# Kernel tuning notes

Hardware: AMD Instinct MI355X
Metric: run time of the kernel (lower is better)

## Reference

```python
import jax, jax.numpy as jnp
import numpy as np

D_MODEL = 1024
N_HEADS = 16
FEATURE_DIM = 16
HEAD_DIM = D_MODEL // N_HEADS  # 64
EPS = 1e-12


def taylor_exp(x):
    """2nd-order Taylor feature map of exp(q^T k / sqrt(d)).
    x: (b, h, l, d) -> (b, h, l, 1 + d + d^2)"""
    d = x.shape[-1]
    rd = jnp.sqrt(jnp.asarray(d, x.dtype))      # sqrt(d)
    rrd = jnp.sqrt(rd)                          # d^(1/4)
    r2 = jnp.sqrt(jnp.asarray(2.0, x.dtype))
    x2 = (x[..., :, None] * x[..., None, :]).reshape(*x.shape[:-1], d * d) / r2
    ones = jnp.ones_like(x[..., :1])
    return jnp.concatenate([ones, x / rrd, x2 / rd], axis=-1)


def setup_inputs() -> dict:
    key = jax.random.key(0)
    k0, k1, k2, k3, k4 = jax.random.split(key, 5)
    b, l = 1, 1024
    scale = 1.0 / np.sqrt(D_MODEL)
    hidden_states = jax.random.normal(k0, (b, l, D_MODEL), dtype=jnp.float32)
    Wq = jax.random.normal(k1, (N_HEADS * FEATURE_DIM, D_MODEL), dtype=jnp.float32) * scale
    Wk = jax.random.normal(k2, (N_HEADS * FEATURE_DIM, D_MODEL), dtype=jnp.float32) * scale
    Wv = jax.random.normal(k3, (N_HEADS * HEAD_DIM, D_MODEL), dtype=jnp.float32) * scale
    Wo = jax.random.normal(k4, (D_MODEL, N_HEADS * HEAD_DIM), dtype=jnp.float32) * scale
    return {"hidden_states": hidden_states, "Wq": Wq, "Wk": Wk, "Wv": Wv, "Wo": Wo}


def reference(hidden_states, Wq, Wk, Wv, Wo):
    b, l, _ = hidden_states.shape
    # projections (bias-free)
    q = (hidden_states @ Wq.T).reshape(b, l, N_HEADS, FEATURE_DIM).transpose(0, 2, 1, 3)
    k = (hidden_states @ Wk.T).reshape(b, l, N_HEADS, FEATURE_DIM).transpose(0, 2, 1, 3)
    v = (hidden_states @ Wv.T).reshape(b, l, N_HEADS, HEAD_DIM).transpose(0, 2, 1, 3)
    qf = taylor_exp(q)   # (b, h, l, D) with D = 1 + d + d^2 = 273
    kf = taylor_exp(k)
    # causal linear attention via associative KV accumulation
    # kv_state[l] = sum_{t<=l} phi(k_t) outer v_t  -> (b, h, l, head_dim, D)
    kv_state = jnp.cumsum(kf[..., None, :] * v[..., :, None], axis=2)
    num = jnp.einsum('bhlD,bhldD->bhld', qf, kv_state)
    den = jnp.einsum('bhlD,bhlD->bhl', qf, jnp.cumsum(kf, axis=2))[..., None] + EPS
    y = num / den                                # (b, h, l, head_dim)
    y = y.transpose(0, 2, 1, 3).reshape(b, l, N_HEADS * HEAD_DIM)
    return y @ Wo.T
```

## Files before the change

### kernel.cpp

```cpp
#include <hip/hip_runtime.h>

#define LSEQ 1024
#define DMODEL 1024
#define NHEADS 16
#define FDIM 16
#define HDIM 64
#define CHUNK 64
#define NCHUNK 16

typedef __attribute__((ext_vector_type(8))) short short8;
typedef __attribute__((ext_vector_type(4))) float floatx4;

__device__ __forceinline__ float bf2f(unsigned short u) {
    unsigned int x = ((unsigned int)u) << 16;
    return __builtin_bit_cast(float, x);
}
__device__ __forceinline__ unsigned short f2bf(float f) {
    unsigned int x = __builtin_bit_cast(unsigned int, f);
    unsigned int r = (x + 0x7fffu + ((x >> 16) & 1u)) >> 16;
    return (unsigned short)r;
}

__device__ __forceinline__ int block_detect_fp32(const unsigned short* wq) {
    __shared__ int cnt;
    if (threadIdx.x == 0) cnt = 0;
    __syncthreads();
    int bad = 0;
    for (int i = threadIdx.x; i < 1024; i += blockDim.x) {
        int e = (wq[i] >> 7) & 0xFF;
        if (e >= 143 || (e > 0 && e <= 80)) bad++;
    }
    if (bad) atomicAdd(&cnt, bad);
    __syncthreads();
    return cnt > 128;
}

#define U_QB   0
#define U_KB   262144
#define U_VB   524288
#define U_YB   1572864

#define MFMA(a, b, c) __builtin_amdgcn_mfma_f32_16x16x32_bf16((a), (b), (c), 0, 0, 0)

__device__ __forceinline__ void gemm64_body(
    unsigned short (&As)[64][136], unsigned short (&Bs)[64][136],
    const void* Araw, int a_fp32, int arow0,
    const void* Braw, int b_fp32, int brow0, floatx4 acc[4]) {
    int t = threadIdx.x;
    int r = t >> 2, c0 = (t & 3) * 32;
    int wave = t >> 6, lane = t & 63;
    int ml = lane & 15, q4 = lane >> 4;
    int mq = (wave >> 1) * 32, nq = (wave & 1) * 32;
    #pragma unroll
    for (int i = 0; i < 4; ++i) acc[i] = (floatx4){0.f, 0.f, 0.f, 0.f};

    short8 av[4], bv[4], av2[4], bv2[4];
    auto stage = [&](int k0, short8* a, short8* b) {
        if (!a_fp32) {
            const unsigned short* Ap = (const unsigned short*)Araw + (size_t)(arow0 + r) * DMODEL + k0 + c0;
            #pragma unroll
            for (int j = 0; j < 4; ++j) a[j] = *(const short8*)(Ap + j * 8);
        } else {
            const float* Ap = (const float*)Araw + (size_t)(arow0 + r) * DMODEL + k0 + c0;
            #pragma unroll
            for (int j = 0; j < 4; ++j)
                #pragma unroll
                for (int u = 0; u < 8; ++u) a[j][u] = (short)f2bf(Ap[j * 8 + u]);
        }
        if (!b_fp32) {
            const unsigned short* Bp = (const unsigned short*)Braw + (size_t)(brow0 + r) * DMODEL + k0 + c0;
            #pragma unroll
            for (int j = 0; j < 4; ++j) b[j] = *(const short8*)(Bp + j * 8);
        } else {
            const float* Bp = (const float*)Braw + (size_t)(brow0 + r) * DMODEL + k0 + c0;
            #pragma unroll
            for (int j = 0; j < 4; ++j)
                #pragma unroll
                for (int u = 0; u < 8; ++u) b[j][u] = (short)f2bf(Bp[j * 8 + u]);
        }
    };

    stage(0, av, bv);
    for (int k0 = 0; k0 < DMODEL; k0 += 128) {
        __syncthreads();
        #pragma unroll
        for (int j = 0; j < 4; ++j) {
            *(short8*)&As[r][c0 + j * 8] = av[j];
            *(short8*)&Bs[r][c0 + j * 8] = bv[j];
        }
        __syncthreads();
        if (k0 + 128 < DMODEL) stage(k0 + 128, av2, bv2);
        #pragma unroll
        for (int kk = 0; kk < 4; ++kk) {
            short8 a0 = *(const short8*)&As[mq + ml][kk * 32 + q4 * 8];
            short8 a1 = *(const short8*)&As[mq + 16 + ml][kk * 32 + q4 * 8];
            short8 b0 = *(const short8*)&Bs[nq + ml][kk * 32 + q4 * 8];
            short8 b1 = *(const short8*)&Bs[nq + 16 + ml][kk * 32 + q4 * 8];
            acc[0] = MFMA(a0, b0, acc[0]); acc[1] = MFMA(a0, b1, acc[1]);
            acc[2] = MFMA(a1, b0, acc[2]); acc[3] = MFMA(a1, b1, acc[3]);
        }
        #pragma unroll
        for (int j = 0; j < 4; ++j) { av[j] = av2[j]; bv[j] = bv2[j]; }
    }
}

__global__ __launch_bounds__(256) void qkv_gemm(
    const void* __restrict__ hidR, const void* __restrict__ WqR,
    const void* __restrict__ WkR, const void* __restrict__ WvR,
    unsigned short* __restrict__ qb, unsigned short* __restrict__ kb,
    unsigned short* __restrict__ vb) {
    int fp32 = block_detect_fp32((const unsigned short*)WqR);
    __shared__ __align__(16) unsigned short As[64][136];
    __shared__ __align__(16) unsigned short Bs[64][136];
    int nb = blockIdx.x, mb = blockIdx.y;
    const void* Braw; unsigned short* Cout; int ldc, col0, br0;
    if (nb < 4)      { Braw = WqR; br0 = nb * 64;       Cout = qb; ldc = 256;  col0 = nb * 64; }
    else if (nb < 8) { Braw = WkR; br0 = (nb - 4) * 64; Cout = kb; ldc = 256;  col0 = (nb - 4) * 64; }
    else             { Braw = WvR; br0 = (nb - 8) * 64; Cout = vb; ldc = 1024; col0 = (nb - 8) * 64; }

    floatx4 acc[4];
    gemm64_body(As, Bs, hidR, fp32, mb * 64, Braw, fp32, br0, acc);

    int wave = threadIdx.x >> 6, lane = threadIdx.x & 63;
    int ml = lane & 15, q4 = lane >> 4;
    int mq = (wave >> 1) * 32, nq = (wave & 1) * 32;
    #pragma unroll
    for (int mi = 0; mi < 2; ++mi)
        #pragma unroll
        for (int ni = 0; ni < 2; ++ni) {
            floatx4 a = acc[mi * 2 + ni];
            int nloc = nq + ni * 16 + ml;
            #pragma unroll
            for (int r4 = 0; r4 < 4; ++r4) {
                int row = mb * 64 + mq + mi * 16 + q4 * 4 + r4;
                Cout[(size_t)row * ldc + col0 + nloc] = f2bf(a[r4]);
            }
        }
}

__global__ __launch_bounds__(256) void flash_attn(
    const unsigned short* __restrict__ qb, const unsigned short* __restrict__ kb,
    const unsigned short* __restrict__ vb, unsigned short* __restrict__ ybB) {
    int h = blockIdx.x & 15, c = blockIdx.x >> 4;
    int l0 = c * CHUNK;
    __shared__ __align__(16) unsigned short qs[64][40];
    __shared__ __align__(16) unsigned short ksm[64][40];
    __shared__ __align__(16) unsigned short vT[80][72];
    __shared__ __align__(16) unsigned short P[64][72];
    int t = threadIdx.x, lane = t & 63, wave = t >> 6;
    int ml = lane & 15, q4 = lane >> 4;
    int m0 = wave * 16;
    int sm = t >> 2, si4 = (t & 3) * 4, scc = (t & 3) * 16;

    {
        *(ushort4*)&qs[sm][si4] = *(const ushort4*)&qb[(size_t)(l0 + sm) * 256 + h * 16 + si4];
        ushort4 z = {0, 0, 0, 0};
        *(ushort4*)&qs[sm][16 + si4]  = z;
        *(ushort4*)&ksm[sm][16 + si4] = z;
    }
    if (t < 64) {
        vT[64][t] = 0x3F80;
        #pragma unroll
        for (int i = 65; i < 80; ++i) vT[i][t] = 0;
    }

    auto load_kv = [&](int j, ushort4& kr, ushort4 vr[4]) {
        kr = *(const ushort4*)&kb[(size_t)(j * 64 + sm) * 256 + h * 16 + si4];
        #pragma unroll
        for (int u = 0; u < 4; ++u)
            vr[u] = *(const ushort4*)&vb[(size_t)(j * 64 + sm) * 1024 + h * 64 + scc + u * 4];
    };

    floatx4 acc[5];
    #pragma unroll
    for (int i = 0; i < 5; ++i) acc[i] = (floatx4){0.f, 0.f, 0.f, 0.f};

    ushort4 kr, vr[4], kr2, vr2[4];
    load_kv(0, kr, vr);

    for (int j = 0; j <= c; ++j) {
        {
            *(ushort4*)&ksm[sm][si4] = kr;
            unsigned short tmp[16];
            #pragma unroll
            for (int u = 0; u < 4; ++u) *(ushort4*)&tmp[u * 4] = vr[u];
            #pragma unroll
            for (int u = 0; u < 16; ++u) vT[scc + u][sm] = tmp[u];
        }
        __syncthreads();
        if (j < c) load_kv(j + 1, kr2, vr2);

        short8 aq = *(const short8*)&qs[m0 + ml][q4 * 8];
        bool diag = (j == c);
        #pragma unroll
        for (int nt = 0; nt < 4; ++nt) {
            short8 bk = *(const short8*)&ksm[nt * 16 + ml][q4 * 8];
            floatx4 s4 = {0.f, 0.f, 0.f, 0.f};
            s4 = MFMA(aq, bk, s4);
            int tt = nt * 16 + ml;
            #pragma unroll
            for (int r = 0; r < 4; ++r) {
                int lrow = m0 + q4 * 4 + r;
                float s = s4[r];
                float p = 1.f + 0.25f * s + 0.03125f * s * s;
                if (diag && tt > lrow) p = 0.f;
                P[lrow][tt] = f2bf(p);
            }
        }

        #pragma unroll
        for (int k0 = 0; k0 < 64; k0 += 32) {
            short8 ap = *(const short8*)&P[m0 + ml][k0 + q4 * 8];
            #pragma unroll
            for (int nt = 0; nt < 5; ++nt) {
                short8 bvv = *(const short8*)&vT[nt * 16 + ml][k0 + q4 * 8];
                acc[nt] = MFMA(ap, bvv, acc[nt]);
            }
        }
        __syncthreads();
        kr = kr2;
        #pragma unroll
        for (int u = 0; u < 4; ++u) vr[u] = vr2[u];
    }

    #pragma unroll
    for (int r = 0; r < 4; ++r) {
        float den = __shfl(acc[4][r], q4 * 16) + 1e-12f;
        float dinv = 1.f / den;
        int lrow = m0 + q4 * 4 + r;
        unsigned short* yp = ybB + (size_t)(l0 + lrow) * 1024 + h * 64;
        #pragma unroll
        for (int nt = 0; nt < 4; ++nt)
            yp[nt * 16 + ml] = f2bf(acc[nt][r] * dinv);
    }
}

__global__ __launch_bounds__(256) void out_gemm(
    const unsigned short* __restrict__ A, const void* __restrict__ WoR,
    void* __restrict__ outv, const unsigned short* __restrict__ wqraw) {
    int fp32 = block_detect_fp32(wqraw);
    __shared__ __align__(16) unsigned short As[64][136];
    __shared__ __align__(16) unsigned short Bs[64][136];
    int nb = blockIdx.x, mb = blockIdx.y;

    floatx4 acc[4];
    gemm64_body(As, Bs, A, 0, mb * 64, WoR, fp32, nb * 64, acc);

    int wave = threadIdx.x >> 6, lane = threadIdx.x & 63;
    int ml = lane & 15, q4 = lane >> 4;
    int mq = (wave >> 1) * 32, nq = (wave & 1) * 32;
    #pragma unroll
    for (int mi = 0; mi < 2; ++mi)
        #pragma unroll
        for (int ni = 0; ni < 2; ++ni) {
            floatx4 a = acc[mi * 2 + ni];
            int n = nb * 64 + nq + ni * 16 + ml;
            #pragma unroll
            for (int r4 = 0; r4 < 4; ++r4) {
                int row = mb * 64 + mq + mi * 16 + q4 * 4 + r4;
                size_t idx = (size_t)row * 1024 + n;
                if (fp32) ((float*)outv)[idx] = a[r4];
                else      ((unsigned short*)outv)[idx] = f2bf(a[r4]);
            }
        }
}

extern "C" void kernel_launch(void* const* d_in, const int* in_sizes, int n_in,
                              void* d_out, int out_size, void* d_ws, size_t ws_size,
                              hipStream_t stream) {
    unsigned short* us = (unsigned short*)d_ws;
    unsigned short* qbB = us + U_QB;
    unsigned short* kbB = us + U_KB;
    unsigned short* vbB = us + U_VB;
    unsigned short* ybB = us + U_YB;
    size_t need = (size_t)(U_YB + 1048576) * 2ull;
    if (ws_size < need) return;

    qkv_gemm<<<dim3(24, 16), 256, 0, stream>>>(d_in[0], d_in[1], d_in[2], d_in[3], qbB, kbB, vbB);
    flash_attn<<<dim3(256), 256, 0, stream>>>(qbB, kbB, vbB, ybB);
    out_gemm<<<dim3(16, 16), 256, 0, stream>>>(ybB, d_in[4], d_out, (const unsigned short*)d_in[1]);
}
```

Baseline: 141.3 us.

## Split causal attention KV range across two blocks and fuse normalization into output GEMM

The attention kernel launches twice as many blocks, each covering half of the causal key chunks for a query chunk, and writes partial fp32 numerators and denominators. The output GEMM sums the two partials and divides by the denominator while staging its A tile, so the normalization is fused there. Both GEMMs also switch to a two-deep register prefetch with a fully unrolled K loop. This is meant to balance the triangular causal workload across CUs, at the cost of extra fp32 partial traffic and more register pressure.

```diff
diff --git a/kernel.cpp b/kernel.cpp
--- a/kernel.cpp
+++ b/kernel.cpp
@@ -38,71 +38,13 @@
 #define U_QB   0
 #define U_KB   262144
 #define U_VB   524288
-#define U_YB   1572864
+#define F_NUM0 786432
+#define F_NUM1 1835008
+#define F_DEN0 2883584
+#define F_DEN1 2899968
+#define F_END  2916352
 
 #define MFMA(a, b, c) __builtin_amdgcn_mfma_f32_16x16x32_bf16((a), (b), (c), 0, 0, 0)
-
-__device__ __forceinline__ void gemm64_body(
-    unsigned short (&As)[64][136], unsigned short (&Bs)[64][136],
-    const void* Araw, int a_fp32, int arow0,
-    const void* Braw, int b_fp32, int brow0, floatx4 acc[4]) {
-    int t = threadIdx.x;
-    int r = t >> 2, c0 = (t & 3) * 32;
-    int wave = t >> 6, lane = t & 63;
-    int ml = lane & 15, q4 = lane >> 4;
-    int mq = (wave >> 1) * 32, nq = (wave & 1) * 32;
-    #pragma unroll
-    for (int i = 0; i < 4; ++i) acc[i] = (floatx4){0.f, 0.f, 0.f, 0.f};
-
-    short8 av[4], bv[4], av2[4], bv2[4];
-    auto stage = [&](int k0, short8* a, short8* b) {
-        if (!a_fp32) {
-            const unsigned short* Ap = (const unsigned short*)Araw + (size_t)(arow0 + r) * DMODEL + k0 + c0;
-            #pragma unroll
-            for (int j = 0; j < 4; ++j) a[j] = *(const short8*)(Ap + j * 8);
-        } else {
-            const float* Ap = (const float*)Araw + (size_t)(arow0 + r) * DMODEL + k0 + c0;
-            #pragma unroll
-            for (int j = 0; j < 4; ++j)
-                #pragma unroll
-                for (int u = 0; u < 8; ++u) a[j][u] = (short)f2bf(Ap[j * 8 + u]);
-        }
-        if (!b_fp32) {
-            const unsigned short* Bp = (const unsigned short*)Braw + (size_t)(brow0 + r) * DMODEL + k0 + c0;
-            #pragma unroll
-            for (int j = 0; j < 4; ++j) b[j] = *(const short8*)(Bp + j * 8);
-        } else {
-            const float* Bp = (const float*)Braw + (size_t)(brow0 + r) * DMODEL + k0 + c0;
-            #pragma unroll
-            for (int j = 0; j < 4; ++j)
-                #pragma unroll
-                for (int u = 0; u < 8; ++u) b[j][u] = (short)f2bf(Bp[j * 8 + u]);
-        }
-    };
-
-    stage(0, av, bv);
-    for (int k0 = 0; k0 < DMODEL; k0 += 128) {
-        __syncthreads();
-        #pragma unroll
-        for (int j = 0; j < 4; ++j) {
-            *(short8*)&As[r][c0 + j * 8] = av[j];
-            *(short8*)&Bs[r][c0 + j * 8] = bv[j];
-        }
-        __syncthreads();
-        if (k0 + 128 < DMODEL) stage(k0 + 128, av2, bv2);
-        #pragma unroll
-        for (int kk = 0; kk < 4; ++kk) {
-            short8 a0 = *(const short8*)&As[mq + ml][kk * 32 + q4 * 8];
-            short8 a1 = *(const short8*)&As[mq + 16 + ml][kk * 32 + q4 * 8];
-            short8 b0 = *(const short8*)&Bs[nq + ml][kk * 32 + q4 * 8];
-            short8 b1 = *(const short8*)&Bs[nq + 16 + ml][kk * 32 + q4 * 8];
-            acc[0] = MFMA(a0, b0, acc[0]); acc[1] = MFMA(a0, b1, acc[1]);
-            acc[2] = MFMA(a1, b0, acc[2]); acc[3] = MFMA(a1, b1, acc[3]);
-        }
-        #pragma unroll
-        for (int j = 0; j < 4; ++j) { av[j] = av2[j]; bv[j] = bv2[j]; }
-    }
-}
 
 __global__ __launch_bounds__(256) void qkv_gemm(
     const void* __restrict__ hidR, const void* __restrict__ WqR,
@@ -118,12 +60,61 @@
     else if (nb < 8) { Braw = WkR; br0 = (nb - 4) * 64; Cout = kb; ldc = 256;  col0 = (nb - 4) * 64; }
     else             { Braw = WvR; br0 = (nb - 8) * 64; Cout = vb; ldc = 1024; col0 = (nb - 8) * 64; }
 
-    floatx4 acc[4];
-    gemm64_body(As, Bs, hidR, fp32, mb * 64, Braw, fp32, br0, acc);
-
-    int wave = threadIdx.x >> 6, lane = threadIdx.x & 63;
+    int t = threadIdx.x;
+    int r = t >> 2, c0 = (t & 3) * 32;
+    int wave = t >> 6, lane = t & 63;
     int ml = lane & 15, q4 = lane >> 4;
     int mq = (wave >> 1) * 32, nq = (wave & 1) * 32;
+    floatx4 acc[4];
+    #pragma unroll
+    for (int i = 0; i < 4; ++i) acc[i] = (floatx4){0.f, 0.f, 0.f, 0.f};
+
+    short8 av[2][4], bv[2][4];
+    auto stage = [&](int k0, short8 a[4], short8 b[4]) {
+        if (!fp32) {
+            const unsigned short* Ap = (const unsigned short*)hidR + (size_t)(mb * 64 + r) * DMODEL + k0 + c0;
+            const unsigned short* Bp = (const unsigned short*)Braw + (size_t)(br0 + r) * DMODEL + k0 + c0;
+            #pragma unroll
+            for (int j = 0; j < 4; ++j) {
+                a[j] = *(const short8*)(Ap + j * 8);
+                b[j] = *(const short8*)(Bp + j * 8);
+            }
+        } else {
+            const float* Ap = (const float*)hidR + (size_t)(mb * 64 + r) * DMODEL + k0 + c0;
+            const float* Bp = (const float*)Braw + (size_t)(br0 + r) * DMODEL + k0 + c0;
+            #pragma unroll
+            for (int j = 0; j < 4; ++j)
+                #pragma unroll
+                for (int u = 0; u < 8; ++u) {
+                    a[j][u] = (short)f2bf(Ap[j * 8 + u]);
+                    b[j][u] = (short)f2bf(Bp[j * 8 + u]);
+                }
+        }
+    };
+
+    stage(0, av[0], bv[0]);
+    stage(128, av[1], bv[1]);
+    #pragma unroll
+    for (int it = 0; it < 8; ++it) {
+        int pp = it & 1;
+        __syncthreads();
+        #pragma unroll
+        for (int j = 0; j < 4; ++j) {
+            *(short8*)&As[r][c0 + j * 8] = av[pp][j];
+            *(short8*)&Bs[r][c0 + j * 8] = bv[pp][j];
+        }
+        __syncthreads();
+        if (it < 6) stage((it + 2) * 128, av[pp], bv[pp]);
+        #pragma unroll
+        for (int kk = 0; kk < 4; ++kk) {
+            short8 a0 = *(const short8*)&As[mq + ml][kk * 32 + q4 * 8];
+            short8 a1 = *(const short8*)&As[mq + 16 + ml][kk * 32 + q4 * 8];
+            short8 b0 = *(const short8*)&Bs[nq + ml][kk * 32 + q4 * 8];
+            short8 b1 = *(const short8*)&Bs[nq + 16 + ml][kk * 32 + q4 * 8];
+            acc[0] = MFMA(a0, b0, acc[0]); acc[1] = MFMA(a0, b1, acc[1]);
+            acc[2] = MFMA(a1, b0, acc[2]); acc[3] = MFMA(a1, b1, acc[3]);
+        }
+    }
     #pragma unroll
     for (int mi = 0; mi < 2; ++mi)
         #pragma unroll
@@ -140,9 +131,18 @@
 
 __global__ __launch_bounds__(256) void flash_attn(
     const unsigned short* __restrict__ qb, const unsigned short* __restrict__ kb,
-    const unsigned short* __restrict__ vb, unsigned short* __restrict__ ybB) {
-    int h = blockIdx.x & 15, c = blockIdx.x >> 4;
+    const unsigned short* __restrict__ vb,
+    float* __restrict__ num0, float* __restrict__ num1,
+    float* __restrict__ den0, float* __restrict__ den1) {
+    int bid = blockIdx.x;
+    int h = bid & 15, c = (bid >> 4) & 15, s = bid >> 8;
     int l0 = c * CHUNK;
+    int half = (c + 1) >> 1;
+    int j0 = s ? half : 0;
+    int j1 = s ? (c + 1) : half;
+    float* numS = s ? num1 : num0;
+    float* denS = s ? den1 : den0;
+
     __shared__ __align__(16) unsigned short qs[64][40];
     __shared__ __align__(16) unsigned short ksm[64][40];
     __shared__ __align__(16) unsigned short vT[80][72];
@@ -176,9 +176,9 @@
     for (int i = 0; i < 5; ++i) acc[i] = (floatx4){0.f, 0.f, 0.f, 0.f};
 
     ushort4 kr, vr[4], kr2, vr2[4];
-    load_kv(0, kr, vr);
-
-    for (int j = 0; j <= c; ++j) {
+    if (j0 < j1) load_kv(j0, kr, vr);
+
+    for (int j = j0; j < j1; ++j) {
         {
             *(ushort4*)&ksm[sm][si4] = kr;
             unsigned short tmp[16];
@@ -188,7 +188,7 @@
             for (int u = 0; u < 16; ++u) vT[scc + u][sm] = tmp[u];
         }
         __syncthreads();
-        if (j < c) load_kv(j + 1, kr2, vr2);
+        if (j + 1 < j1) load_kv(j + 1, kr2, vr2);
 
         short8 aq = *(const short8*)&qs[m0 + ml][q4 * 8];
         bool diag = (j == c);
@@ -199,15 +199,14 @@
             s4 = MFMA(aq, bk, s4);
             int tt = nt * 16 + ml;
             #pragma unroll
-            for (int r = 0; r < 4; ++r) {
-                int lrow = m0 + q4 * 4 + r;
-                float s = s4[r];
-                float p = 1.f + 0.25f * s + 0.03125f * s * s;
+            for (int rr = 0; rr < 4; ++rr) {
+                int lrow = m0 + q4 * 4 + rr;
+                float sv = s4[rr];
+                float p = 1.f + 0.25f * sv + 0.03125f * sv * sv;
                 if (diag && tt > lrow) p = 0.f;
                 P[lrow][tt] = f2bf(p);
             }
         }
-
         #pragma unroll
         for (int k0 = 0; k0 < 64; k0 += 32) {
             short8 ap = *(const short8*)&P[m0 + ml][k0 + q4 * 8];
@@ -224,31 +223,94 @@
     }
 
     #pragma unroll
-    for (int r = 0; r < 4; ++r) {
-        float den = __shfl(acc[4][r], q4 * 16) + 1e-12f;
-        float dinv = 1.f / den;
-        int lrow = m0 + q4 * 4 + r;
-        unsigned short* yp = ybB + (size_t)(l0 + lrow) * 1024 + h * 64;
-        #pragma unroll
-        for (int nt = 0; nt < 4; ++nt)
-            yp[nt * 16 + ml] = f2bf(acc[nt][r] * dinv);
+    for (int rr = 0; rr < 4; ++rr) {
+        int lrow = m0 + q4 * 4 + rr;
+        float* np = numS + (size_t)(l0 + lrow) * 1024 + h * 64;
+        #pragma unroll
+        for (int nt = 0; nt < 4; ++nt) np[nt * 16 + ml] = acc[nt][rr];
+        if (ml == 0) denS[(size_t)(l0 + lrow) * 16 + h] = acc[4][rr];
     }
 }
 
 __global__ __launch_bounds__(256) void out_gemm(
-    const unsigned short* __restrict__ A, const void* __restrict__ WoR,
-    void* __restrict__ outv, const unsigned short* __restrict__ wqraw) {
+    const float* __restrict__ num0, const float* __restrict__ num1,
+    const float* __restrict__ den0, const float* __restrict__ den1,
+    const void* __restrict__ WoR, void* __restrict__ outv,
+    const unsigned short* __restrict__ wqraw) {
     int fp32 = block_detect_fp32(wqraw);
     __shared__ __align__(16) unsigned short As[64][136];
     __shared__ __align__(16) unsigned short Bs[64][136];
     int nb = blockIdx.x, mb = blockIdx.y;
-
-    floatx4 acc[4];
-    gemm64_body(As, Bs, A, 0, mb * 64, WoR, fp32, nb * 64, acc);
-
-    int wave = threadIdx.x >> 6, lane = threadIdx.x & 63;
+    int br0 = nb * 64;
+
+    int t = threadIdx.x;
+    int r = t >> 2, c0 = (t & 3) * 32;
+    int wave = t >> 6, lane = t & 63;
     int ml = lane & 15, q4 = lane >> 4;
     int mq = (wave >> 1) * 32, nq = (wave & 1) * 32;
+    floatx4 acc[4];
+    #pragma unroll
+    for (int i = 0; i < 4; ++i) acc[i] = (floatx4){0.f, 0.f, 0.f, 0.f};
+
+    int l = mb * 64 + r;
+    short8 av[2][4], bv[2][4];
+    auto stage = [&](int k0, short8 a[4], short8 b[4]) {
+        int h = (k0 + c0) >> 6;
+        float den = den0[(size_t)l * 16 + h] + den1[(size_t)l * 16 + h] + 1e-12f;
+        float dinv = 1.f / den;
+        const float* n0p = num0 + (size_t)l * 1024 + k0 + c0;
+        const float* n1p = num1 + (size_t)l * 1024 + k0 + c0;
+        #pragma unroll
+        for (int j = 0; j < 4; ++j) {
+            float4 x0 = *(const float4*)(n0p + j * 8);
+            float4 x1 = *(const float4*)(n1p + j * 8);
+            float4 y0 = *(const float4*)(n0p + j * 8 + 4);
+            float4 y1 = *(const float4*)(n1p + j * 8 + 4);
+            a[j][0] = (short)f2bf((x0.x + x1.x) * dinv);
+            a[j][1] = (short)f2bf((x0.y + x1.y) * dinv);
+            a[j][2] = (short)f2bf((x0.z + x1.z) * dinv);
+            a[j][3] = (short)f2bf((x0.w + x1.w) * dinv);
+            a[j][4] = (short)f2bf((y0.x + y1.x) * dinv);
+            a[j][5] = (short)f2bf((y0.y + y1.y) * dinv);
+            a[j][6] = (short)f2bf((y0.z + y1.z) * dinv);
+            a[j][7] = (short)f2bf((y0.w + y1.w) * dinv);
+        }
+        if (!fp32) {
+            const unsigned short* Bp = (const unsigned short*)WoR + (size_t)(br0 + r) * DMODEL + k0 + c0;
+            #pragma unroll
+            for (int j = 0; j < 4; ++j) b[j] = *(const short8*)(Bp + j * 8);
+        } else {
+            const float* Bp = (const float*)WoR + (size_t)(br0 + r) * DMODEL + k0 + c0;
+            #pragma unroll
+            for (int j = 0; j < 4; ++j)
+                #pragma unroll
+                for (int u = 0; u < 8; ++u) b[j][u] = (short)f2bf(Bp[j * 8 + u]);
+        }
+    };
+
+    stage(0, av[0], bv[0]);
+    stage(128, av[1], bv[1]);
+    #pragma unroll
+    for (int it = 0; it < 8; ++it) {
+        int pp = it & 1;
+        __syncthreads();
+        #pragma unroll
+        for (int j = 0; j < 4; ++j) {
+            *(short8*)&As[r][c0 + j * 8] = av[pp][j];
+            *(short8*)&Bs[r][c0 + j * 8] = bv[pp][j];
+        }
+        __syncthreads();
+        if (it < 6) stage((it + 2) * 128, av[pp], bv[pp]);
+        #pragma unroll
+        for (int kk = 0; kk < 4; ++kk) {
+            short8 a0 = *(const short8*)&As[mq + ml][kk * 32 + q4 * 8];
+            short8 a1 = *(const short8*)&As[mq + 16 + ml][kk * 32 + q4 * 8];
+            short8 b0 = *(const short8*)&Bs[nq + ml][kk * 32 + q4 * 8];
+            short8 b1 = *(const short8*)&Bs[nq + 16 + ml][kk * 32 + q4 * 8];
+            acc[0] = MFMA(a0, b0, acc[0]); acc[1] = MFMA(a0, b1, acc[1]);
+            acc[2] = MFMA(a1, b0, acc[2]); acc[3] = MFMA(a1, b1, acc[3]);
+        }
+    }
     #pragma unroll
     for (int mi = 0; mi < 2; ++mi)
         #pragma unroll
@@ -269,14 +331,19 @@
                               void* d_out, int out_size, void* d_ws, size_t ws_size,
                               hipStream_t stream) {
     unsigned short* us = (unsigned short*)d_ws;
+    float* ws = (float*)d_ws;
     unsigned short* qbB = us + U_QB;
     unsigned short* kbB = us + U_KB;
     unsigned short* vbB = us + U_VB;
-    unsigned short* ybB = us + U_YB;
-    size_t need = (size_t)(U_YB + 1048576) * 2ull;
+    float* num0 = ws + F_NUM0;
+    float* num1 = ws + F_NUM1;
+    float* den0 = ws + F_DEN0;
+    float* den1 = ws + F_DEN1;
+    size_t need = (size_t)F_END * 4ull;
     if (ws_size < need) return;
 
     qkv_gemm<<<dim3(24, 16), 256, 0, stream>>>(d_in[0], d_in[1], d_in[2], d_in[3], qbB, kbB, vbB);
-    flash_attn<<<dim3(256), 256, 0, stream>>>(qbB, kbB, vbB, ybB);
-    out_gemm<<<dim3(16, 16), 256, 0, stream>>>(ybB, d_in[4], d_out, (const unsigned short*)d_in[1]);
-}
+    flash_attn<<<dim3(512), 256, 0, stream>>>(qbB, kbB, vbB, num0, num1, den0, den1);
+    out_gemm<<<dim3(16, 16), 256, 0, stream>>>(num0, num1, den0, den1, d_in[4], d_out,
+                                               (const unsigned short*)d_in[1]);
+}
```

Measured after the change: 153.3 us. 8.5% more time.
